# Kernel tuning notes

Measured on AMD Instinct MI355X. Metric: run time of the kernel, lower is better.

## Reference

```python
import jax, jax.numpy as jnp
import numpy as np

TOP_K = 2

def setup_inputs() -> dict:
    key = jax.random.key(0)
    k1, k2 = jax.random.split(key)
    T, D, E = 16384, 2048, 64  # num_tokens, d_model, num_experts
    x = jax.random.normal(k1, (T, D), dtype=jnp.float32)
    Wg = jax.random.normal(k2, (D, E), dtype=jnp.float32) / np.sqrt(D)
    return {"x": x, "Wg": Wg}

def reference(x, Wg):
    T, E = x.shape[0], Wg.shape[1]
    # gate logits + softmax over experts
    logits = x @ Wg                                   # [T, E]
    probs = jax.nn.softmax(logits, axis=-1)           # [T, E]
    # top-k expert selection, renormalize selected weights
    top_vals, top_idx = jax.lax.top_k(probs, TOP_K)   # [T, K]
    top_vals = top_vals / jnp.sum(top_vals, axis=-1, keepdims=True)
    # scatter sparse gate weights into dense [T, E]
    rows = jnp.arange(T)[:, None]                     # [T, 1]
    gate_weights = jnp.zeros_like(probs).at[rows, top_idx].set(top_vals)
    # load-balance aux loss: E * sum_e f_e * P_e
    mask = jnp.sum(jax.nn.one_hot(top_idx, E, dtype=probs.dtype), axis=1)  # [T, E]
    f = jnp.mean(mask, axis=0)    # fraction of tokens routed to each expert
    P = jnp.mean(probs, axis=0)   # mean router prob per expert
    aux_loss = E * jnp.sum(f * P)
    return gate_weights, top_idx, aux_loss
```

## Files before the change

kernel.cpp:

```cpp
#include <hip/hip_runtime.h>


typedef __attribute__((ext_vector_type(8))) _Float16 half8;
typedef __attribute__((ext_vector_type(4))) float f32x4;

constexpr int DD   = 2048;
constexpr int EE   = 64;
constexpr int BM   = 16;
constexpr int BK   = 64;
constexpr int NCH  = DD / BK;

#define BAR()   asm volatile("s_barrier" ::: "memory")
#define WVM(N)  asm volatile("s_waitcnt vmcnt(" #N ")" ::: "memory")

__global__ __launch_bounds__(256) void wsplit_kernel(
    const float* __restrict__ Wg, _Float16* __restrict__ whTc,
    _Float16* __restrict__ wlTc)
{
    __shared__ float xl[64][68];
    const int tid = threadIdx.x;
    const int kc  = blockIdx.x;
    const int k0  = kc * 64;

#pragma unroll
    for (int r = 0; r < 4; ++r) {
        int slot = tid + r * 256;
        int row = slot >> 4, c4 = (slot & 15) << 2;
        *(float4*)&xl[row][c4] = *(const float4*)&Wg[(size_t)(k0 + row) * EE + c4];
    }
    __syncthreads();

    const int n  = tid >> 2;
    const int kq = tid & 3;
    _Float16 hh[16], ll[16];
#pragma unroll
    for (int i = 0; i < 16; ++i) {
        float v = xl[kq * 16 + i][n];
        _Float16 h = (_Float16)v;
        hh[i] = h;
        ll[i] = (_Float16)((v - (float)h) * 4096.f);
    }
    const size_t rb = (size_t)kc * 4096 + n * 64;
#pragma unroll
    for (int j = 0; j < 2; ++j) {
        int bp  = kq * 2 + j;
        int pos = (bp ^ (n & 7)) * 8;
        *(half8*)&whTc[rb + pos] = *(const half8*)&hh[j * 8];
        *(half8*)&wlTc[rb + pos] = *(const half8*)&ll[j * 8];
    }
}

__global__ __launch_bounds__(256, 4) void gate_kernel(
    const float* __restrict__ x, const _Float16* __restrict__ whTc,
    const _Float16* __restrict__ wlTc,
    float* __restrict__ gate_out, float* __restrict__ idx_out,
    float* __restrict__ pSum, float* __restrict__ pCnt)
{
    __shared__ __align__(16) union {
        struct {
            float    xs[2][BM][BK];
            _Float16 wsb[2][2][EE][BK];
        } st;
        struct { float logits[2][BM][68]; float auxsm[2][4][64]; } ep;
    } sm;

    const int tid  = threadIdx.x;
    const int wv   = tid >> 6;
    const int lane = tid & 63;
    const int kh   = wv & 1;
    const int nh   = wv >> 1;
    const size_t tok0 = (size_t)blockIdx.x * BM;

    auto stage = [&](int buf, int c) {
        {
            int slot = tid;
            int row  = slot >> 4;
            int cb   = (slot & 15) << 4;
            int sb   = cb ^ ((row & 7) << 5);
            __builtin_amdgcn_global_load_lds(
                x + (tok0 + row) * DD + c * BK + (sb >> 2),
                &sm.st.xs[buf][row][(slot & 15) << 2], 16, 0, 0);
        }
#pragma unroll
        for (int p = 0; p < 2; ++p) {
            const _Float16* wg = (p ? wlTc : whTc) + (size_t)c * 4096;
            _Float16* dst = &sm.st.wsb[buf][p][0][0];
#pragma unroll
            for (int r = 0; r < 2; ++r) {
                int slot = tid + r * 256;
                __builtin_amdgcn_global_load_lds(
                    wg + slot * 8, dst + slot * 8, 16, 0, 0);
            }
        }
    };

    f32x4 accH0 = {0.f,0.f,0.f,0.f}, accL0 = {0.f,0.f,0.f,0.f};
    f32x4 accH1 = {0.f,0.f,0.f,0.f}, accL1 = {0.f,0.f,0.f,0.f};

    const int arow = lane & 15;
    const int kg   = lane >> 4;
    const int k8   = kh * 32 + kg * 8;
    const int ax   = k8 ^ ((arow & 7) << 3);
    const int e0   = nh * 32 + (lane & 15);
    const int e1   = e0 + 16;
    const int b0   = k8 ^ ((e0 & 7) << 3);
    const int b1   = k8 ^ ((e1 & 7) << 3);

    auto compute = [&](int buf) {
        float4 xa = *(const float4*)&sm.st.xs[buf][arow][ax];
        float4 xb = *(const float4*)&sm.st.xs[buf][arow][ax + 4];
        half8 ah, al;
#define CVT(E, V)                                                              \
        { _Float16 h = (_Float16)(V); ah[E] = h;                               \
          al[E] = (_Float16)(((V) - (float)h) * 4096.f); }
        CVT(0, xa.x) CVT(1, xa.y) CVT(2, xa.z) CVT(3, xa.w)
        CVT(4, xb.x) CVT(5, xb.y) CVT(6, xb.z) CVT(7, xb.w)
#undef CVT
        half8 bh0 = *(const half8*)&sm.st.wsb[buf][0][e0][b0];
        half8 bl0 = *(const half8*)&sm.st.wsb[buf][1][e0][b0];
        half8 bh1 = *(const half8*)&sm.st.wsb[buf][0][e1][b1];
        half8 bl1 = *(const half8*)&sm.st.wsb[buf][1][e1][b1];
        accH0 = __builtin_amdgcn_mfma_f32_16x16x32_f16(ah, bh0, accH0, 0, 0, 0);
        accL0 = __builtin_amdgcn_mfma_f32_16x16x32_f16(ah, bl0, accL0, 0, 0, 0);
        accL0 = __builtin_amdgcn_mfma_f32_16x16x32_f16(al, bh0, accL0, 0, 0, 0);
        accH1 = __builtin_amdgcn_mfma_f32_16x16x32_f16(ah, bh1, accH1, 0, 0, 0);
        accL1 = __builtin_amdgcn_mfma_f32_16x16x32_f16(ah, bl1, accL1, 0, 0, 0);
        accL1 = __builtin_amdgcn_mfma_f32_16x16x32_f16(al, bh1, accL1, 0, 0, 0);
    };

    stage(0, 0);
    stage(1, 1);
    WVM(5); BAR();

#pragma unroll 1
    for (int c = 0; c < NCH; ++c) {
        const int buf = c & 1;
        compute(buf);
        BAR();
        if (c + 2 < NCH)       { stage(buf, c + 2); WVM(5); }
        else if (c + 2 == NCH) { WVM(0); }
        BAR();
    }

    __syncthreads();
    const float inv = 1.f / 4096.f;
#pragma unroll
    for (int e = 0; e < 4; ++e) {
        const int row = (lane >> 4) * 4 + e;
        sm.ep.logits[kh][row][e0] = accH0[e] + accL0[e] * inv;
        sm.ep.logits[kh][row][e1] = accH1[e] + accL1[e] * inv;
    }
    __syncthreads();

    float sumP_acc = 0.f;
    float cnt_acc  = 0.f;
#pragma unroll 1
    for (int tt = 0; tt < 4; ++tt) {
        const int tl = wv * 4 + tt;
        const size_t t = tok0 + tl;
        float v = sm.ep.logits[0][tl][lane] + sm.ep.logits[1][tl][lane];

        float m = v;
#pragma unroll
        for (int off = 32; off; off >>= 1) m = fmaxf(m, __shfl_xor(m, off, 64));
        float p = expf(v - m);
        float s = p;
#pragma unroll
        for (int off = 32; off; off >>= 1) s += __shfl_xor(s, off, 64);
        float prob = p / s;
        sumP_acc += prob;

        float bv = prob; int bi = lane;
#pragma unroll
        for (int off = 32; off; off >>= 1) {
            float ov = __shfl_xor(bv, off, 64);
            int   oi = __shfl_xor(bi, off, 64);
            if (ov > bv || (ov == bv && oi < bi)) { bv = ov; bi = oi; }
        }
        float v2 = (lane == bi) ? -1.f : prob;
        float bv2 = v2; int bi2 = lane;
#pragma unroll
        for (int off = 32; off; off >>= 1) {
            float ov = __shfl_xor(bv2, off, 64);
            int   oi = __shfl_xor(bi2, off, 64);
            if (ov > bv2 || (ov == bv2 && oi < bi2)) { bv2 = ov; bi2 = oi; }
        }

        float denom = bv + bv2;
        float g1 = bv / denom, g2 = bv2 / denom;
        float g = (lane == bi) ? g1 : ((lane == bi2) ? g2 : 0.f);
        gate_out[t * EE + lane] = g;
        if (lane == 0) {
            idx_out[2 * t]     = (float)bi;
            idx_out[2 * t + 1] = (float)bi2;
        }
        cnt_acc += (lane == bi)  ? 1.f : 0.f;
        cnt_acc += (lane == bi2) ? 1.f : 0.f;
    }

    sm.ep.auxsm[0][wv][lane] = sumP_acc;
    sm.ep.auxsm[1][wv][lane] = cnt_acc;
    __syncthreads();
    if (wv == 0) {
        float sp = 0.f, c2 = 0.f;
#pragma unroll
        for (int w = 0; w < 4; ++w) {
            sp += sm.ep.auxsm[0][w][lane];
            c2 += sm.ep.auxsm[1][w][lane];
        }
        pSum[(size_t)blockIdx.x * 64 + lane] = sp;
        pCnt[(size_t)blockIdx.x * 64 + lane] = c2;
    }
}

__global__ __launch_bounds__(1024) void aux_kernel(
    const float* __restrict__ pSum, const float* __restrict__ pCnt,
    float* __restrict__ aux_out, int nblocks, float scale)
{
    const int tid  = threadIdx.x;
    const int wv   = tid >> 6;
    const int lane = tid & 63;
    __shared__ float smem[2][16][64];

    float sp[4] = {0.f, 0.f, 0.f, 0.f};
    float cc[4] = {0.f, 0.f, 0.f, 0.f};
    for (int b = wv * 4; b < nblocks; b += 64) {
#pragma unroll
        for (int u = 0; u < 4; ++u) {
            sp[u] += pSum[(size_t)(b + u) * 64 + lane];
            cc[u] += pCnt[(size_t)(b + u) * 64 + lane];
        }
    }
    smem[0][wv][lane] = (sp[0] + sp[1]) + (sp[2] + sp[3]);
    smem[1][wv][lane] = (cc[0] + cc[1]) + (cc[2] + cc[3]);
    __syncthreads();
    if (wv == 0) {
        float SP = 0.f, C = 0.f;
#pragma unroll
        for (int w = 0; w < 16; ++w) {
            SP += smem[0][w][lane];
            C  += smem[1][w][lane];
        }
        float prod = SP * C;
#pragma unroll
        for (int off = 32; off; off >>= 1) prod += __shfl_xor(prod, off, 64);
        if (lane == 0) aux_out[0] = prod * scale;
    }
}

extern "C" void kernel_launch(void* const* d_in, const int* in_sizes, int n_in,
                              void* d_out, int out_size, void* d_ws, size_t ws_size,
                              hipStream_t stream) {
    const float* x  = (const float*)d_in[0];
    const float* Wg = (const float*)d_in[1];
    const int T = in_sizes[0] / DD;

    float* out      = (float*)d_out;
    float* gate_out = out;
    float* idx_out  = out + (size_t)T * EE;
    float* aux_out  = idx_out + (size_t)T * 2;

    const int nblocks = T / BM;
    _Float16* whTc = (_Float16*)d_ws;
    _Float16* wlTc = whTc + (size_t)EE * DD;
    float* pSum = (float*)(wlTc + (size_t)EE * DD);
    float* pCnt = pSum + (size_t)nblocks * 64;

    wsplit_kernel<<<DD / 64, 256, 0, stream>>>(Wg, whTc, wlTc);
    gate_kernel<<<nblocks, 256, 0, stream>>>(x, whTc, wlTc,
                                             gate_out, idx_out, pSum, pCnt);

    const float scale = (float)EE / ((float)T * (float)T);
    aux_kernel<<<1, 1024, 0, stream>>>(pSum, pCnt, aux_out, nblocks, scale);
}
```

Before: 55.82 us.

## Give each wave private LDS staging buffers and drop block-wide barriers in K loop

```diff
diff --git a/kernel.cpp b/kernel.cpp
--- a/kernel.cpp
+++ b/kernel.cpp
@@ -10,20 +10,20 @@
 constexpr int BK   = 64;
 constexpr int NCH  = DD / BK;
 
-#define BAR()   asm volatile("s_barrier" ::: "memory")
 #define WVM(N)  asm volatile("s_waitcnt vmcnt(" #N ")" ::: "memory")
 
 __global__ __launch_bounds__(256) void wsplit_kernel(
-    const float* __restrict__ Wg, _Float16* __restrict__ whTc,
-    _Float16* __restrict__ wlTc)
+    const float* __restrict__ Wg, _Float16* __restrict__ whT2,
+    _Float16* __restrict__ wlT2)
 {
-    __shared__ float xl[64][68];
+    __shared__ float xl[32][65];
     const int tid = threadIdx.x;
-    const int kc  = blockIdx.x;
-    const int k0  = kc * 64;
-
-#pragma unroll
-    for (int r = 0; r < 4; ++r) {
+    const int kc  = blockIdx.x >> 1;
+    const int kh  = blockIdx.x & 1;
+    const int k0  = kc * 64 + kh * 32;
+
+#pragma unroll
+    for (int r = 0; r < 2; ++r) {
         int slot = tid + r * 256;
         int row = slot >> 4, c4 = (slot & 15) << 2;
         *(float4*)&xl[row][c4] = *(const float4*)&Wg[(size_t)(k0 + row) * EE + c4];
@@ -31,35 +31,30 @@
     __syncthreads();
 
     const int n  = tid >> 2;
-    const int kq = tid & 3;
-    _Float16 hh[16], ll[16];
-#pragma unroll
-    for (int i = 0; i < 16; ++i) {
-        float v = xl[kq * 16 + i][n];
+    const int bq = tid & 3;
+    _Float16 hh[8], ll[8];
+#pragma unroll
+    for (int j = 0; j < 8; ++j) {
+        float v = xl[bq * 8 + j][n];
         _Float16 h = (_Float16)v;
-        hh[i] = h;
-        ll[i] = (_Float16)((v - (float)h) * 4096.f);
-    }
-    const size_t rb = (size_t)kc * 4096 + n * 64;
-#pragma unroll
-    for (int j = 0; j < 2; ++j) {
-        int bp  = kq * 2 + j;
-        int pos = (bp ^ (n & 7)) * 8;
-        *(half8*)&whTc[rb + pos] = *(const half8*)&hh[j * 8];
-        *(half8*)&wlTc[rb + pos] = *(const half8*)&ll[j * 8];
-    }
+        hh[j] = h;
+        ll[j] = (_Float16)((v - (float)h) * 4096.f);
+    }
+    const size_t base = ((size_t)(kc * 2 + kh) * 64 + n) * 32 + (bq ^ (n & 3)) * 8;
+    *(half8*)&whT2[base] = *(const half8*)&hh[0];
+    *(half8*)&wlT2[base] = *(const half8*)&ll[0];
 }
 
 __global__ __launch_bounds__(256, 4) void gate_kernel(
-    const float* __restrict__ x, const _Float16* __restrict__ whTc,
-    const _Float16* __restrict__ wlTc,
+    const float* __restrict__ x, const _Float16* __restrict__ whT2,
+    const _Float16* __restrict__ wlT2,
     float* __restrict__ gate_out, float* __restrict__ idx_out,
     float* __restrict__ pSum, float* __restrict__ pCnt)
 {
     __shared__ __align__(16) union {
         struct {
-            float    xs[2][BM][BK];
-            _Float16 wsb[2][2][EE][BK];
+            float    xs[4][2][16][32];
+            _Float16 wsb[4][2][2][32][32];
         } st;
         struct { float logits[2][BM][68]; float auxsm[2][4][64]; } ep;
     } sm;
@@ -72,24 +67,25 @@
     const size_t tok0 = (size_t)blockIdx.x * BM;
 
     auto stage = [&](int buf, int c) {
-        {
-            int slot = tid;
-            int row  = slot >> 4;
-            int cb   = (slot & 15) << 4;
-            int sb   = cb ^ ((row & 7) << 5);
+        const float* xg = x + tok0 * DD + c * BK + kh * 32;
+#pragma unroll
+        for (int r = 0; r < 2; ++r) {
+            int s   = lane + r * 64;
+            int row = s >> 3, q = s & 7;
+            int qs  = q ^ ((row & 3) << 1);
             __builtin_amdgcn_global_load_lds(
-                x + (tok0 + row) * DD + c * BK + (sb >> 2),
-                &sm.st.xs[buf][row][(slot & 15) << 2], 16, 0, 0);
-        }
+                xg + (size_t)row * DD + qs * 4,
+                &sm.st.xs[wv][buf][row][q * 4], 16, 0, 0);
+        }
+        const size_t wbase = ((size_t)(c * 2 + kh) * 64 + nh * 32) * 32;
 #pragma unroll
         for (int p = 0; p < 2; ++p) {
-            const _Float16* wg = (p ? wlTc : whTc) + (size_t)c * 4096;
-            _Float16* dst = &sm.st.wsb[buf][p][0][0];
+            const _Float16* wg = (p ? wlT2 : whT2) + wbase;
+            _Float16* dst = &sm.st.wsb[wv][buf][p][0][0];
 #pragma unroll
             for (int r = 0; r < 2; ++r) {
-                int slot = tid + r * 256;
-                __builtin_amdgcn_global_load_lds(
-                    wg + slot * 8, dst + slot * 8, 16, 0, 0);
+                int s = lane + r * 64;
+                __builtin_amdgcn_global_load_lds(wg + s * 8, dst + s * 8, 16, 0, 0);
             }
         }
     };
@@ -99,16 +95,14 @@
 
     const int arow = lane & 15;
     const int kg   = lane >> 4;
-    const int k8   = kh * 32 + kg * 8;
-    const int ax   = k8 ^ ((arow & 7) << 3);
-    const int e0   = nh * 32 + (lane & 15);
-    const int e1   = e0 + 16;
-    const int b0   = k8 ^ ((e0 & 7) << 3);
-    const int b1   = k8 ^ ((e1 & 7) << 3);
+    const int fidx = (kg ^ (arow & 3)) * 8;
+    const int wsl  = (kg ^ (arow & 3)) * 8;
+    const int e0l  = arow;
+    const int e1l  = arow + 16;
 
     auto compute = [&](int buf) {
-        float4 xa = *(const float4*)&sm.st.xs[buf][arow][ax];
-        float4 xb = *(const float4*)&sm.st.xs[buf][arow][ax + 4];
+        float4 xa = *(const float4*)&sm.st.xs[wv][buf][arow][fidx];
+        float4 xb = *(const float4*)&sm.st.xs[wv][buf][arow][fidx + 4];
         half8 ah, al;
 #define CVT(E, V)                                                              \
         { _Float16 h = (_Float16)(V); ah[E] = h;                               \
@@ -116,10 +110,10 @@
         CVT(0, xa.x) CVT(1, xa.y) CVT(2, xa.z) CVT(3, xa.w)
         CVT(4, xb.x) CVT(5, xb.y) CVT(6, xb.z) CVT(7, xb.w)
 #undef CVT
-        half8 bh0 = *(const half8*)&sm.st.wsb[buf][0][e0][b0];
-        half8 bl0 = *(const half8*)&sm.st.wsb[buf][1][e0][b0];
-        half8 bh1 = *(const half8*)&sm.st.wsb[buf][0][e1][b1];
-        half8 bl1 = *(const half8*)&sm.st.wsb[buf][1][e1][b1];
+        half8 bh0 = *(const half8*)&sm.st.wsb[wv][buf][0][e0l][wsl];
+        half8 bl0 = *(const half8*)&sm.st.wsb[wv][buf][1][e0l][wsl];
+        half8 bh1 = *(const half8*)&sm.st.wsb[wv][buf][0][e1l][wsl];
+        half8 bl1 = *(const half8*)&sm.st.wsb[wv][buf][1][e1l][wsl];
         accH0 = __builtin_amdgcn_mfma_f32_16x16x32_f16(ah, bh0, accH0, 0, 0, 0);
         accL0 = __builtin_amdgcn_mfma_f32_16x16x32_f16(ah, bl0, accL0, 0, 0, 0);
         accL0 = __builtin_amdgcn_mfma_f32_16x16x32_f16(al, bh0, accL0, 0, 0, 0);
@@ -130,25 +124,23 @@
 
     stage(0, 0);
     stage(1, 1);
-    WVM(5); BAR();
-
 #pragma unroll 1
-    for (int c = 0; c < NCH; ++c) {
+    for (int c = 0; c < NCH - 1; ++c) {
         const int buf = c & 1;
+        WVM(6);
         compute(buf);
-        BAR();
-        if (c + 2 < NCH)       { stage(buf, c + 2); WVM(5); }
-        else if (c + 2 == NCH) { WVM(0); }
-        BAR();
-    }
+        if (c + 2 < NCH) stage(buf, c + 2);
+    }
+    WVM(0);
+    compute((NCH - 1) & 1);
 
     __syncthreads();
     const float inv = 1.f / 4096.f;
 #pragma unroll
     for (int e = 0; e < 4; ++e) {
         const int row = (lane >> 4) * 4 + e;
-        sm.ep.logits[kh][row][e0] = accH0[e] + accL0[e] * inv;
-        sm.ep.logits[kh][row][e1] = accH1[e] + accL1[e] * inv;
+        sm.ep.logits[kh][row][nh * 32 + e0l] = accH0[e] + accL0[e] * inv;
+        sm.ep.logits[kh][row][nh * 32 + e1l] = accH1[e] + accL1[e] * inv;
     }
     __syncthreads();
 
@@ -261,13 +253,13 @@
     float* aux_out  = idx_out + (size_t)T * 2;
 
     const int nblocks = T / BM;
-    _Float16* whTc = (_Float16*)d_ws;
-    _Float16* wlTc = whTc + (size_t)EE * DD;
-    float* pSum = (float*)(wlTc + (size_t)EE * DD);
+    _Float16* whT2 = (_Float16*)d_ws;
+    _Float16* wlT2 = whT2 + (size_t)EE * DD;
+    float* pSum = (float*)(wlT2 + (size_t)EE * DD);
     float* pCnt = pSum + (size_t)nblocks * 64;
 
-    wsplit_kernel<<<DD / 64, 256, 0, stream>>>(Wg, whTc, wlTc);
-    gate_kernel<<<nblocks, 256, 0, stream>>>(x, whTc, wlTc,
+    wsplit_kernel<<<64, 256, 0, stream>>>(Wg, whT2, wlT2);
+    gate_kernel<<<nblocks, 256, 0, stream>>>(x, whT2, wlT2,
                                              gate_out, idx_out, pSum, pCnt);
 
     const float scale = (float)EE / ((float)T * (float)T);
```

Result: slower. 72.60 us (+30.1%).
